# Performance work log

Measured on AMD Instinct MI355X. Metric: run time of the kernel, lower is better.

Reference implementation:

```python
import jax, jax.numpy as jnp
import numpy as np

T, B, IN_DIM = 2048, 8, 512
D_VALUE, D_KEY = 512, 128
CHUNK = 128
EPS = 1e-8


def setup_inputs() -> dict:
    key = jax.random.key(0)
    ks = jax.random.split(key, 9)
    s = 0.02
    return {
        "x": jax.random.normal(ks[0], (T, B, IN_DIM), dtype=jnp.float32),
        "Wv": jax.random.normal(ks[1], (D_VALUE, IN_DIM), dtype=jnp.float32) * s,
        "bv": jnp.zeros((D_VALUE,), dtype=jnp.float32),
        "Wk": jax.random.normal(ks[2], (D_KEY, IN_DIM), dtype=jnp.float32) * s,
        "bk": jnp.zeros((D_KEY,), dtype=jnp.float32),
        "Wq": jax.random.normal(ks[3], (D_KEY, IN_DIM), dtype=jnp.float32) * s,
        "bq": jnp.zeros((D_KEY,), dtype=jnp.float32),
        "Wa": jax.random.normal(ks[4], (D_KEY, IN_DIM), dtype=jnp.float32) * s,
        "ba": jnp.zeros((D_KEY,), dtype=jnp.float32),
    }


def _gla_forward(x, Wv, bv, Wk, bk, Wq, bq, Wa, ba):
    # Projections: x (T,B,in) -> v (T,B,d), k/q/alpha (T,B,n)
    v = jnp.einsum("tbi,di->tbd", x, Wv) + bv
    k = jnp.einsum("tbi,ni->tbn", x, Wk) + bk
    q = jnp.einsum("tbi,ni->tbn", x, Wq) + bq
    alpha = jax.nn.sigmoid(jnp.einsum("tbi,ni->tbn", x, Wa) + ba)

    Tt, Bb, d = v.shape
    n = k.shape[2]
    nch = Tt // CHUNK  # T chosen divisible by CHUNK

    # Reshape time-major tensors into (n_chunks, C, B, dim)
    v_r = v.reshape(nch, CHUNK, Bb, d)
    k_r = k.reshape(nch, CHUNK, Bb, n)
    q_r = q.reshape(nch, CHUNK, Bb, n)
    a_r = alpha.reshape(nch, CHUNK, Bb, n)

    def chunk_step(S_prev, inp):
        v_ch, k_ch, q_ch, a_ch = inp  # (C,B,d), (C,B,n), (C,B,n), (C,B,n)
        outer = jnp.einsum("tbd,tbn->tbdn", v_ch, k_ch)  # (C,B,d,n)
        cp = jnp.cumprod(jnp.maximum(a_ch, EPS), axis=0)  # (C,B,n)
        inv_prefix = 1.0 / (cp + EPS)
        scaled = jnp.cumsum(outer * inv_prefix[:, :, None, :], axis=0)
        # local decayed state plus carried state decayed by prefix product
        S_local = (scaled + S_prev[None, :, :, :]) * cp[:, :, None, :]
        y_ch = jnp.einsum("tbdn,tbn->tbd", S_local, q_ch)  # S @ q
        return S_local[-1], y_ch

    S0 = jnp.zeros((Bb, d, n), dtype=v.dtype)
    _, y = jax.lax.scan(chunk_step, S0, (v_r, k_r, q_r, a_r))
    return y.reshape(Tt, Bb, d)


def reference(x, Wv, bv, Wk, bk, Wq, bq, Wa, ba):
    return _gla_forward(x, Wv, bv, Wk, bk, Wq, bq, Wa, ba)
```

## Files before the change

kernel.cpp:

```cpp
#include <hip/hip_runtime.h>


#define EPSV 1e-8f

typedef __bf16 bf16x8 __attribute__((ext_vector_type(8)));
typedef __bf16 bf16x4 __attribute__((ext_vector_type(4)));
typedef float f32x4 __attribute__((ext_vector_type(4)));

__device__ __forceinline__ void async_copy16(const void* g, void* l) {
  __builtin_amdgcn_global_load_lds(
      (const __attribute__((address_space(1))) void*)g,
      (__attribute__((address_space(3))) void*)l, 16, 0, 0);
}

__global__ __launch_bounds__(256) void conv_bf16(const float* __restrict__ src,
                                                 __bf16* __restrict__ dst) {
  long i = ((long)blockIdx.x * 256 + threadIdx.x) * 8;
  float4 f0 = *(const float4*)(src + i);
  float4 f1 = *(const float4*)(src + i + 4);
  bf16x8 h;
  h[0] = (__bf16)f0.x; h[1] = (__bf16)f0.y; h[2] = (__bf16)f0.z; h[3] = (__bf16)f0.w;
  h[4] = (__bf16)f1.x; h[5] = (__bf16)f1.y; h[6] = (__bf16)f1.z; h[7] = (__bf16)f1.w;
  *(bf16x8*)(dst + i) = h;
}

__global__ __launch_bounds__(256) void conv_w(const float* __restrict__ Wv,
                                              const float* __restrict__ Wk,
                                              const float* __restrict__ Wq,
                                              const float* __restrict__ Wa,
                                              __bf16* __restrict__ dst) {
  long i = ((long)blockIdx.x * 256 + threadIdx.x) * 8;
  int row = (int)(i >> 9);
  int col = (int)(i & 511);
  const float* src;
  if (row < 512)      src = Wv + (long)row * 512 + col;
  else if (row < 640) src = Wk + (long)(row - 512) * 512 + col;
  else if (row < 768) src = Wq + (long)(row - 640) * 512 + col;
  else                src = Wa + (long)(row - 768) * 512 + col;
  float4 f0 = *(const float4*)(src);
  float4 f1 = *(const float4*)(src + 4);
  bf16x8 h;
  h[0] = (__bf16)f0.x; h[1] = (__bf16)f0.y; h[2] = (__bf16)f0.z; h[3] = (__bf16)f0.w;
  h[4] = (__bf16)f1.x; h[5] = (__bf16)f1.y; h[6] = (__bf16)f1.z; h[7] = (__bf16)f1.w;
  *(bf16x8*)(dst + i) = h;
}

__global__ __launch_bounds__(256) void proj_mfma(
    const __bf16* __restrict__ xb, const __bf16* __restrict__ wcat,
    const float* __restrict__ bv, const float* __restrict__ bk,
    const float* __restrict__ bq, const float* __restrict__ ba,
    __bf16* __restrict__ vt, __bf16* __restrict__ kout,
    __bf16* __restrict__ qout, float* __restrict__ aout) {
  __shared__ __attribute__((aligned(16))) char smem[128 * 136 * 2];
  __bf16* a_sm = (__bf16*)smem;
  __bf16* b_sm = a_sm + 128 * 64;
  __bf16* tr   = (__bf16*)smem;

  int tid = threadIdx.x;
  int lane = tid & 63, wave = tid >> 6;
  int mt = blockIdx.x, nt = blockIdx.y;
  int wr = wave >> 1, wcol = wave & 1;

  const __bf16* xtile = xb + (long)mt * 128 * 512;
  const __bf16* wtile = wcat + (long)nt * 128 * 512;

  f32x4 acc[4][4] = {};
  int lr8 = lane >> 3, lc8 = lane & 7;
  int l15 = lane & 15, qd = lane >> 4;
  int slsrc = (lc8 ^ lr8) * 8;
  int frd = l15 & 7;

  for (int k0 = 0; k0 < 512; k0 += 64) {
#pragma unroll
    for (int h = 0; h < 4; ++h) {
      int q = wave * 4 + h;
      int row = q * 8 + lr8;
      async_copy16(xtile + (long)row * 512 + k0 + slsrc, &a_sm[q * 512]);
      async_copy16(wtile + (long)row * 512 + k0 + slsrc, &b_sm[q * 512]);
    }
    __syncthreads();
#pragma unroll
    for (int kk = 0; kk < 2; ++kk) {
      bf16x8 af[4], bfr[4];
#pragma unroll
      for (int t = 0; t < 4; ++t) {
        int ra = wr * 64 + t * 16 + l15;
        int rb = wcol * 64 + t * 16 + l15;
        int slot = ((kk * 4 + qd) ^ frd) * 8;
        af[t]  = *(const bf16x8*)&a_sm[ra * 64 + slot];
        bfr[t] = *(const bf16x8*)&b_sm[rb * 64 + slot];
      }
#pragma unroll
      for (int i = 0; i < 4; ++i)
#pragma unroll
        for (int j = 0; j < 4; ++j)
          acc[i][j] = __builtin_amdgcn_mfma_f32_16x16x32_bf16(af[i], bfr[j], acc[i][j], 0, 0, 0);
    }
    __syncthreads();
  }

  if (nt < 4) {
    const float* bias = bv + nt * 128;
#pragma unroll
    for (int i = 0; i < 4; ++i)
#pragma unroll
      for (int j = 0; j < 4; ++j) {
        int col = wcol * 64 + j * 16 + l15;
        float bz = bias[col];
#pragma unroll
        for (int r = 0; r < 4; ++r) {
          int row = wr * 64 + i * 16 + qd * 4 + r;
          tr[col * 136 + (row & 7) * 16 + (row >> 3)] = (__bf16)(acc[i][j][r] + bz);
        }
      }
    __syncthreads();
    int cbase = (mt >> 3) * 8;
    int s0 = (mt & 7) * 16;
#pragma unroll
    for (int it = 0; it < 4; ++it) {
      int p = it * 256 + tid;
      int d = p & 127, b = p >> 7;
      bf16x8 u0 = *(const bf16x8*)&tr[d * 136 + b * 16];
      bf16x8 u1 = *(const bf16x8*)&tr[d * 136 + b * 16 + 8];
      __bf16* dst = vt + ((long)(cbase + b) * 512 + nt * 128 + d) * 128 + s0;
      *(bf16x8*)dst = u0;
      *(bf16x8*)(dst + 8) = u1;
    }
    return;
  }

  const float* bias; bool sig = false;
  __bf16* dstb = nullptr; float* dstf = nullptr;
  if (nt == 4)      { bias = bk; dstb = kout; }
  else if (nt == 5) { bias = bq; dstb = qout; }
  else              { bias = ba; dstf = aout; sig = true; }

#pragma unroll
  for (int i = 0; i < 4; ++i)
#pragma unroll
    for (int j = 0; j < 4; ++j) {
      int col = wcol * 64 + j * 16 + l15;
      float bz = bias[col];
#pragma unroll
      for (int r = 0; r < 4; ++r) {
        int row = wr * 64 + i * 16 + qd * 4 + r;
        float z = acc[i][j][r] + bz;
        long addr = ((long)mt * 128 + row) * 128 + col;
        if (sig) dstf[addr] = 1.f / (1.f + __expf(-z));
        else     dstb[addr] = (__bf16)z;
      }
    }
}

__global__ __launch_bounds__(512) void scan_cp(const float* __restrict__ a,
                                               const __bf16* __restrict__ k,
                                               const __bf16* __restrict__ q,
                                               __bf16* __restrict__ kbs,
                                               __bf16* __restrict__ qb,
                                               __bf16* __restrict__ kt,
                                               float* __restrict__ cpend) {
  __shared__ float segprod[8][64];
  int tid = threadIdx.x;
  int nl = tid & 63;
  int seg = tid >> 6;
  int bid = blockIdx.x;
  int nh = bid & 1;
  int b = (bid >> 1) & 7;
  int c = bid >> 4;
  int n = nh * 64 + nl;
  long base = ((long)c * 1024 + b) * 128 + n;
  int t0 = seg * 16;

  float av[16];
  float p = 1.f;
#pragma unroll
  for (int i = 0; i < 16; ++i) {
    float v = fmaxf(a[base + (long)(t0 + i) * 1024], EPSV);
    av[i] = v;
    p *= v;
  }
  segprod[seg][nl] = p;
  __syncthreads();

  float prefix = 1.f;
#pragma unroll
  for (int s = 0; s < 7; ++s)
    if (s < seg) prefix *= segprod[s][nl];
  if (seg == 7) cpend[(c * 8 + b) * 128 + n] = prefix * p;

  float cp = prefix;
  __bf16 ktbuf[16];
#pragma unroll
  for (int i = 0; i < 16; ++i) {
    long off = base + (long)(t0 + i) * 1024;
    cp *= av[i];
    float kk = (float)k[off] / (cp + EPSV);
    float qq = (float)q[off] * cp;
    __bf16 kh = (__bf16)kk;
    kbs[off] = kh;
    qb[off] = (__bf16)qq;
    ktbuf[i] = kh;
  }
  __bf16* dst = kt + ((long)((c * 8 + b) * 128 + n)) * 128 + t0;
#pragma unroll
  for (int i = 0; i < 2; ++i) {
    bf16x8 h;
#pragma unroll
    for (int j = 0; j < 8; ++j) h[j] = ktbuf[i * 8 + j];
    *(bf16x8*)(dst + i * 8) = h;
  }
}

__global__ __launch_bounds__(256) void gmm(const __bf16* __restrict__ vt,
                                           const __bf16* __restrict__ kt,
                                           const float* __restrict__ cpend,
                                           __bf16* __restrict__ Gt) {
  int tid = threadIdx.x, lane = tid & 63, wave = tid >> 6;
  int wr = wave >> 1, wc = wave & 1;
  int l15 = lane & 15, qd = lane >> 4;
  int cb = blockIdx.x >> 2, dt = blockIdx.x & 3;
  const __bf16* vbase = vt + ((long)cb * 512 + dt * 128) * 128;
  const __bf16* kbase = kt + (long)cb * 16384;
  f32x4 acc[4][4] = {};
#pragma unroll
  for (int kk = 0; kk < 4; ++kk) {
    int k0 = kk * 32;
    bf16x8 af[4], bfr[4];
#pragma unroll
    for (int i = 0; i < 4; ++i)
      af[i] = *(const bf16x8*)(vbase + (long)(wr * 64 + i * 16 + l15) * 128 + k0 + qd * 8);
#pragma unroll
    for (int j = 0; j < 4; ++j)
      bfr[j] = *(const bf16x8*)(kbase + (long)(wc * 64 + j * 16 + l15) * 128 + k0 + qd * 8);
#pragma unroll
    for (int i = 0; i < 4; ++i)
#pragma unroll
      for (int j = 0; j < 4; ++j)
        acc[i][j] = __builtin_amdgcn_mfma_f32_16x16x32_bf16(af[i], bfr[j], acc[i][j], 0, 0, 0);
  }
  float ce[4];
#pragma unroll
  for (int j = 0; j < 4; ++j) ce[j] = cpend[cb * 128 + wc * 64 + j * 16 + l15];
#pragma unroll
  for (int i = 0; i < 4; ++i)
#pragma unroll
    for (int j = 0; j < 4; ++j) {
      int col = wc * 64 + j * 16 + l15;
#pragma unroll
      for (int r = 0; r < 4; ++r) {
        int row = wr * 64 + i * 16 + qd * 4 + r;
        Gt[((long)cb * 512 + dt * 128 + row) * 128 + col] = (__bf16)(acc[i][j][r] * ce[j]);
      }
    }
}

__global__ __launch_bounds__(256) void scan_state(const __bf16* __restrict__ Gt,
                                                  const float* __restrict__ cpend,
                                                  __bf16* __restrict__ St) {
  long e = ((long)blockIdx.x * 256 + threadIdx.x) * 4;
  int n0 = (int)(e & 127);
  int b = (int)(e >> 16);
  float4 S = {0.f, 0.f, 0.f, 0.f};
#pragma unroll
  for (int c = 0; c < 16; ++c) {
    long idx = (long)c * 524288 + e;
    bf16x4 g = *(const bf16x4*)(Gt + idx);
    bf16x4 sv;
    sv[0] = (__bf16)S.x; sv[1] = (__bf16)S.y;
    sv[2] = (__bf16)S.z; sv[3] = (__bf16)S.w;
    *(bf16x4*)(St + idx) = sv;
    const float4 cp = *(const float4*)(cpend + (c * 8 + b) * 128 + n0);
    S.x = (float)g[0] + S.x * cp.x;
    S.y = (float)g[1] + S.y * cp.y;
    S.z = (float)g[2] + S.z * cp.z;
    S.w = (float)g[3] + S.w * cp.w;
  }
}

__global__ __launch_bounds__(256) void ymm(const __bf16* __restrict__ qb,
                                           const __bf16* __restrict__ kbs,
                                           const __bf16* __restrict__ vt,
                                           const __bf16* __restrict__ St,
                                           float* __restrict__ out) {
  __shared__ __bf16 A_lds[128 * 136];
  int tid = threadIdx.x, lane = tid & 63, wave = tid >> 6;
  int wr = wave >> 1, wc = wave & 1;
  int l15 = lane & 15, qd = lane >> 4;
  int cb = blockIdx.x >> 2, dt = blockIdx.x & 3;
  int c = cb >> 3, b = cb & 7;
  const __bf16* qbase = qb + ((long)c * 1024 + b) * 128;
  const __bf16* kbase = kbs + ((long)c * 1024 + b) * 128;

  {
    f32x4 accA[4][4] = {};
#pragma unroll
    for (int kk = 0; kk < 4; ++kk) {
      int k0 = kk * 32;
      bf16x8 af[4], bfr[4];
#pragma unroll
      for (int i = 0; i < 4; ++i)
        af[i] = *(const bf16x8*)(qbase + (long)(wr * 64 + i * 16 + l15) * 1024 + k0 + qd * 8);
#pragma unroll
      for (int j = 0; j < 4; ++j)
        bfr[j] = *(const bf16x8*)(kbase + (long)(wc * 64 + j * 16 + l15) * 1024 + k0 + qd * 8);
#pragma unroll
      for (int i = 0; i < 4; ++i)
#pragma unroll
        for (int j = 0; j < 4; ++j)
          accA[i][j] = __builtin_amdgcn_mfma_f32_16x16x32_bf16(af[i], bfr[j], accA[i][j], 0, 0, 0);
    }
#pragma unroll
    for (int i = 0; i < 4; ++i)
#pragma unroll
      for (int j = 0; j < 4; ++j) {
        int s = wc * 64 + j * 16 + l15;
#pragma unroll
        for (int r = 0; r < 4; ++r) {
          int t = wr * 64 + i * 16 + qd * 4 + r;
          A_lds[t * 136 + s] = (s <= t) ? (__bf16)accA[i][j][r] : (__bf16)0.f;
        }
      }
  }
  __syncthreads();

  f32x4 acc[4][4] = {};
  const __bf16* vbase = vt + ((long)cb * 512 + dt * 128) * 128;
  const __bf16* sbase = St + ((long)cb * 512 + dt * 128) * 128;
#pragma unroll
  for (int kk = 0; kk < 4; ++kk) {
    int k0 = kk * 32;
    bf16x8 af[4], bfr[4];
#pragma unroll
    for (int i = 0; i < 4; ++i)
      af[i] = *(const bf16x8*)(vbase + (long)(wr * 64 + i * 16 + l15) * 128 + k0 + qd * 8);
#pragma unroll
    for (int j = 0; j < 4; ++j)
      bfr[j] = *(const bf16x8*)&A_lds[(wc * 64 + j * 16 + l15) * 136 + k0 + qd * 8];
#pragma unroll
    for (int i = 0; i < 4; ++i)
#pragma unroll
      for (int j = 0; j < 4; ++j)
        acc[i][j] = __builtin_amdgcn_mfma_f32_16x16x32_bf16(af[i], bfr[j], acc[i][j], 0, 0, 0);
  }
#pragma unroll
  for (int kk = 0; kk < 4; ++kk) {
    int k0 = kk * 32;
    bf16x8 af[4], bfr[4];
#pragma unroll
    for (int i = 0; i < 4; ++i)
      af[i] = *(const bf16x8*)(sbase + (long)(wr * 64 + i * 16 + l15) * 128 + k0 + qd * 8);
#pragma unroll
    for (int j = 0; j < 4; ++j)
      bfr[j] = *(const bf16x8*)(qbase + (long)(wc * 64 + j * 16 + l15) * 1024 + k0 + qd * 8);
#pragma unroll
    for (int i = 0; i < 4; ++i)
#pragma unroll
      for (int j = 0; j < 4; ++j)
        acc[i][j] = __builtin_amdgcn_mfma_f32_16x16x32_bf16(af[i], bfr[j], acc[i][j], 0, 0, 0);
  }

#pragma unroll
  for (int i = 0; i < 4; ++i)
#pragma unroll
    for (int j = 0; j < 4; ++j) {
      int colt = wc * 64 + j * 16 + l15;
      long addr = ((long)(c * 128 + colt) * 8 + b) * 512 + dt * 128 + wr * 64 + i * 16 + qd * 4;
      *(float4*)(out + addr) = *(float4*)&acc[i][j];
    }
}

extern "C" void kernel_launch(void* const* d_in, const int* in_sizes, int n_in,
                              void* d_out, int out_size, void* d_ws, size_t ws_size,
                              hipStream_t stream) {
  const float* x  = (const float*)d_in[0];
  const float* Wv = (const float*)d_in[1];
  const float* bv = (const float*)d_in[2];
  const float* Wk = (const float*)d_in[3];
  const float* bk = (const float*)d_in[4];
  const float* Wq = (const float*)d_in[5];
  const float* bq = (const float*)d_in[6];
  const float* Wa = (const float*)d_in[7];
  const float* ba = (const float*)d_in[8];
  float* out = (float*)d_out;
  float* ws = (float*)d_ws;

  float*  a_buf = ws;
  __bf16* qb    = (__bf16*)(ws + 2097152);
  __bf16* kbs   = (__bf16*)(ws + 3145728);
  __bf16* kt    = (__bf16*)(ws + 4194304);
  __bf16* vt    = (__bf16*)(ws + 5242880);
  __bf16* k_raw = (__bf16*)(ws + 9437184);
  __bf16* q_raw = (__bf16*)(ws + 10485760);
  __bf16* xb    = (__bf16*)(ws + 11534336);
  __bf16* Wcat  = (__bf16*)(ws + 15728640);
  __bf16* Gt    = xb;
  __bf16* St    = (__bf16*)(ws + 15958016);
  float*  cpend = ws + 20152320;

  conv_bf16<<<4096, 256, 0, stream>>>(x, xb);
  conv_w<<<224, 256, 0, stream>>>(Wv, Wk, Wq, Wa, Wcat);
  proj_mfma<<<dim3(128, 7), 256, 0, stream>>>(xb, Wcat, bv, bk, bq, ba,
                                              vt, k_raw, q_raw, a_buf);
  scan_cp<<<256, 512, 0, stream>>>(a_buf, k_raw, q_raw, kbs, qb, kt, cpend);
  gmm<<<512, 256, 0, stream>>>(vt, kt, cpend, Gt);
  scan_state<<<512, 256, 0, stream>>>(Gt, cpend, St);
  ymm<<<512, 256, 0, stream>>>(qb, kbs, vt, St, out);
}
```

Baseline: 183.2 us.

## Stage GEMM operands in XOR-swizzled LDS via async global-to-LDS copies

The gmm and ymm kernels now copy their full 128x128 operand tiles from global memory into shared memory with async global_load_lds copies, using an XOR swizzle so fragment reads avoid bank conflicts. MFMA fragments are then read from LDS instead of issuing repeated strided global loads, and q is reused from LDS for both of its uses in ymm. In exchange the kernels use much more LDS (about 100KB in ymm), which lowers occupancy, and ymm adds extra barriers that serialise loads with compute.

```diff
diff --git a/kernel.cpp b/kernel.cpp
--- a/kernel.cpp
+++ b/kernel.cpp
@@ -215,23 +215,40 @@
                                            const __bf16* __restrict__ kt,
                                            const float* __restrict__ cpend,
                                            __bf16* __restrict__ Gt) {
+  __shared__ __attribute__((aligned(16))) __bf16 v_sm[128 * 128];
+  __shared__ __attribute__((aligned(16))) __bf16 k_sm[128 * 128];
   int tid = threadIdx.x, lane = tid & 63, wave = tid >> 6;
   int wr = wave >> 1, wc = wave & 1;
   int l15 = lane & 15, qd = lane >> 4;
   int cb = blockIdx.x >> 2, dt = blockIdx.x & 3;
   const __bf16* vbase = vt + ((long)cb * 512 + dt * 128) * 128;
   const __bf16* kbase = kt + (long)cb * 16384;
+
+  int rowoff = lane >> 4, sl = lane & 15;
+#pragma unroll
+  for (int it = 0; it < 8; ++it) {
+    int rbase = it * 16 + wave * 4;
+    int row = rbase + rowoff;
+    int sg = (sl ^ (row & 15)) * 8;
+    async_copy16(vbase + (long)row * 128 + sg, &v_sm[rbase * 128]);
+    async_copy16(kbase + (long)row * 128 + sg, &k_sm[rbase * 128]);
+  }
+  __syncthreads();
+
   f32x4 acc[4][4] = {};
 #pragma unroll
   for (int kk = 0; kk < 4; ++kk) {
-    int k0 = kk * 32;
     bf16x8 af[4], bfr[4];
 #pragma unroll
-    for (int i = 0; i < 4; ++i)
-      af[i] = *(const bf16x8*)(vbase + (long)(wr * 64 + i * 16 + l15) * 128 + k0 + qd * 8);
-#pragma unroll
-    for (int j = 0; j < 4; ++j)
-      bfr[j] = *(const bf16x8*)(kbase + (long)(wc * 64 + j * 16 + l15) * 128 + k0 + qd * 8);
+    for (int i = 0; i < 4; ++i) {
+      int ra = wr * 64 + i * 16 + l15;
+      af[i] = *(const bf16x8*)&v_sm[ra * 128 + (((kk * 4 + qd) ^ l15) & 15) * 8];
+    }
+#pragma unroll
+    for (int j = 0; j < 4; ++j) {
+      int rb = wc * 64 + j * 16 + l15;
+      bfr[j] = *(const bf16x8*)&k_sm[rb * 128 + (((kk * 4 + qd) ^ l15) & 15) * 8];
+    }
 #pragma unroll
     for (int i = 0; i < 4; ++i)
 #pragma unroll
@@ -282,27 +299,45 @@
                                            const __bf16* __restrict__ vt,
                                            const __bf16* __restrict__ St,
                                            float* __restrict__ out) {
-  __shared__ __bf16 A_lds[128 * 136];
+  __shared__ __attribute__((aligned(16))) __bf16 q_sm[128 * 128];
+  __shared__ __attribute__((aligned(16))) __bf16 x_sm[128 * 128];
+  __shared__ __attribute__((aligned(16))) __bf16 A_lds[128 * 136];
   int tid = threadIdx.x, lane = tid & 63, wave = tid >> 6;
   int wr = wave >> 1, wc = wave & 1;
   int l15 = lane & 15, qd = lane >> 4;
   int cb = blockIdx.x >> 2, dt = blockIdx.x & 3;
   int c = cb >> 3, b = cb & 7;
-  const __bf16* qbase = qb + ((long)c * 1024 + b) * 128;
-  const __bf16* kbase = kbs + ((long)c * 1024 + b) * 128;
+  const __bf16* qg = qb + ((long)c * 1024 + b) * 128;
+  const __bf16* kg = kbs + ((long)c * 1024 + b) * 128;
+  const __bf16* vbase = vt + ((long)cb * 512 + dt * 128) * 128;
+  const __bf16* sbase = St + ((long)cb * 512 + dt * 128) * 128;
+
+  int rowoff = lane >> 4, sl = lane & 15;
+#pragma unroll
+  for (int it = 0; it < 8; ++it) {
+    int rbase = it * 16 + wave * 4;
+    int row = rbase + rowoff;
+    int sg = (sl ^ (row & 15)) * 8;
+    async_copy16(qg + (long)row * 1024 + sg, &q_sm[rbase * 128]);
+    async_copy16(kg + (long)row * 1024 + sg, &x_sm[rbase * 128]);
+  }
+  __syncthreads();
 
   {
     f32x4 accA[4][4] = {};
 #pragma unroll
     for (int kk = 0; kk < 4; ++kk) {
-      int k0 = kk * 32;
       bf16x8 af[4], bfr[4];
 #pragma unroll
-      for (int i = 0; i < 4; ++i)
-        af[i] = *(const bf16x8*)(qbase + (long)(wr * 64 + i * 16 + l15) * 1024 + k0 + qd * 8);
-#pragma unroll
-      for (int j = 0; j < 4; ++j)
-        bfr[j] = *(const bf16x8*)(kbase + (long)(wc * 64 + j * 16 + l15) * 1024 + k0 + qd * 8);
+      for (int i = 0; i < 4; ++i) {
+        int ra = wr * 64 + i * 16 + l15;
+        af[i] = *(const bf16x8*)&q_sm[ra * 128 + (((kk * 4 + qd) ^ l15) & 15) * 8];
+      }
+#pragma unroll
+      for (int j = 0; j < 4; ++j) {
+        int rb = wc * 64 + j * 16 + l15;
+        bfr[j] = *(const bf16x8*)&x_sm[rb * 128 + (((kk * 4 + qd) ^ l15) & 15) * 8];
+      }
 #pragma unroll
       for (int i = 0; i < 4; ++i)
 #pragma unroll
@@ -323,16 +358,25 @@
   }
   __syncthreads();
 
+#pragma unroll
+  for (int it = 0; it < 8; ++it) {
+    int rbase = it * 16 + wave * 4;
+    int row = rbase + rowoff;
+    int sg = (sl ^ (row & 15)) * 8;
+    async_copy16(vbase + (long)row * 128 + sg, &x_sm[rbase * 128]);
+  }
+  __syncthreads();
+
   f32x4 acc[4][4] = {};
-  const __bf16* vbase = vt + ((long)cb * 512 + dt * 128) * 128;
-  const __bf16* sbase = St + ((long)cb * 512 + dt * 128) * 128;
 #pragma unroll
   for (int kk = 0; kk < 4; ++kk) {
     int k0 = kk * 32;
     bf16x8 af[4], bfr[4];
 #pragma unroll
-    for (int i = 0; i < 4; ++i)
-      af[i] = *(const bf16x8*)(vbase + (long)(wr * 64 + i * 16 + l15) * 128 + k0 + qd * 8);
+    for (int i = 0; i < 4; ++i) {
+      int ra = wr * 64 + i * 16 + l15;
+      af[i] = *(const bf16x8*)&x_sm[ra * 128 + (((kk * 4 + qd) ^ l15) & 15) * 8];
+    }
 #pragma unroll
     for (int j = 0; j < 4; ++j)
       bfr[j] = *(const bf16x8*)&A_lds[(wc * 64 + j * 16 + l15) * 136 + k0 + qd * 8];
@@ -342,16 +386,30 @@
       for (int j = 0; j < 4; ++j)
         acc[i][j] = __builtin_amdgcn_mfma_f32_16x16x32_bf16(af[i], bfr[j], acc[i][j], 0, 0, 0);
   }
+  __syncthreads();
+
+#pragma unroll
+  for (int it = 0; it < 8; ++it) {
+    int rbase = it * 16 + wave * 4;
+    int row = rbase + rowoff;
+    int sg = (sl ^ (row & 15)) * 8;
+    async_copy16(sbase + (long)row * 128 + sg, &x_sm[rbase * 128]);
+  }
+  __syncthreads();
+
 #pragma unroll
   for (int kk = 0; kk < 4; ++kk) {
-    int k0 = kk * 32;
     bf16x8 af[4], bfr[4];
 #pragma unroll
-    for (int i = 0; i < 4; ++i)
-      af[i] = *(const bf16x8*)(sbase + (long)(wr * 64 + i * 16 + l15) * 128 + k0 + qd * 8);
-#pragma unroll
-    for (int j = 0; j < 4; ++j)
-      bfr[j] = *(const bf16x8*)(qbase + (long)(wc * 64 + j * 16 + l15) * 1024 + k0 + qd * 8);
+    for (int i = 0; i < 4; ++i) {
+      int ra = wr * 64 + i * 16 + l15;
+      af[i] = *(const bf16x8*)&x_sm[ra * 128 + (((kk * 4 + qd) ^ l15) & 15) * 8];
+    }
+#pragma unroll
+    for (int j = 0; j < 4; ++j) {
+      int rb = wc * 64 + j * 16 + l15;
+      bfr[j] = *(const bf16x8*)&q_sm[rb * 128 + (((kk * 4 + qd) ^ l15) & 15) * 8];
+    }
 #pragma unroll
     for (int i = 0; i < 4; ++i)
 #pragma unroll
```

Result: faster. 178.4 us (-2.6%).
